# Kernel optimization log

Hardware: AMD Instinct MI355X
Metric: run time of the kernel (lower is better)

Reference implementation:

```python
import jax, jax.numpy as jnp
import numpy as np

B, S, F = 4, 2048, 64
HID, D, H = 256, 128, 8
DK = D // H


def _mlp_params(key, fan_in, hid, out):
    k1, k2, k3, k4 = jax.random.split(key, 4)
    s1 = 1.0 / np.sqrt(fan_in)
    s2 = 1.0 / np.sqrt(hid)
    return (
        jax.random.uniform(k1, (fan_in, hid), jnp.float32, -s1, s1),
        jax.random.uniform(k2, (hid,), jnp.float32, -s1, s1),
        jax.random.uniform(k3, (hid, out), jnp.float32, -s2, s2),
        jax.random.uniform(k4, (out,), jnp.float32, -s2, s2),
    )


def setup_inputs() -> dict:
    key = jax.random.key(0)
    kx, kq, kk, kv = jax.random.split(key, 4)
    qW1, qb1, qW2, qb2 = _mlp_params(kq, F, HID, D)
    kW1, kb1, kW2, kb2 = _mlp_params(kk, F, HID, D)
    vW1, vb1, vW2, vb2 = _mlp_params(kv, F, HID, D)
    return {
        "x": jax.random.normal(kx, (B, S, F), jnp.float32),
        "qW1": qW1, "qb1": qb1, "qW2": qW2, "qb2": qb2,
        "kW1": kW1, "kb1": kb1, "kW2": kW2, "kb2": kb2,
        "vW1": vW1, "vb1": vb1, "vW2": vW2, "vb2": vb2,
    }


def _mlp(x, W1, b1, W2, b2):
    h = jax.nn.elu(x @ W1 + b1)
    return h @ W2 + b2


def reference(x, qW1, qb1, qW2, qb2, kW1, kb1, kW2, kb2, vW1, vb1, vW2, vb2):
    b = x.shape[0]
    q = _mlp(x, qW1, qb1, qW2, qb2).reshape(b, -1, H, DK)  # [B,S,H,dk]
    k = _mlp(x, kW1, kb1, kW2, kb2).reshape(b, -1, H, DK)
    v = _mlp(x, vW1, vb1, vW2, vb2).reshape(b, -1, H, DK)
    scores = jnp.einsum("bqhd,bkhd->bhqk", q, k) / np.sqrt(DK).astype(np.float32)
    attn = jax.nn.softmax(scores, axis=-1)
    out = jnp.einsum("bhqk,bkhd->bqhd", attn, v).reshape(b, -1, D)  # [B,S,D]
    return jnp.max(out, axis=1)  # [B,D]
```

## Files before the change

kernel.cpp:

```cpp
#include <hip/hip_runtime.h>
#include <hip/hip_bf16.h>
#include <math.h>
#include <string.h>

#define BB 4
#define SS 2048
#define FF 64
#define HID 256
#define DD 128
#define HH 8
#define DK 16
#define NROWS (BB*SS)
#define MROWS 32
#define QPB 64
#define NQB (SS/QPB)
#define KSPLIT 4
#define KRANGE (SS/KSPLIT)
#define XSTR 72
#define HSTR 264
#define VROWS 17

#define QSCALE 0.3606737602222409f

typedef __attribute__((ext_vector_type(8))) short short8;
typedef __attribute__((ext_vector_type(16))) float float16v;

static __device__ __forceinline__ unsigned pk_bf16(float a, float b) {
    __hip_bfloat16 ha = __float2bfloat16(a), hb = __float2bfloat16(b);
    unsigned short lo, hi;
    memcpy(&lo, &ha, 2); memcpy(&hi, &hb, 2);
    return ((unsigned)hi << 16) | (unsigned)lo;
}
static __device__ __forceinline__ unsigned trunc_pk(float a, float b) {
    return __builtin_amdgcn_perm(__float_as_uint(b), __float_as_uint(a), 0x07060302u);
}

__global__ __launch_bounds__(256) void convert_kernel(
    const float* __restrict__ qW1, const float* __restrict__ kW1, const float* __restrict__ vW1,
    const float* __restrict__ qW2, const float* __restrict__ kW2, const float* __restrict__ vW2,
    __hip_bfloat16* __restrict__ W1T, __hip_bfloat16* __restrict__ W2T)
{
    const int m = blockIdx.x;
    const int quarter = blockIdx.y;
    const int t = threadIdx.x;
    if (m < 3) {
        const float* src = (m == 0) ? qW1 : (m == 1) ? kW1 : vW1;
        __hip_bfloat16* dst = W1T + (size_t)m * (FF * HID);
        const int c = t;
        for (int k0 = quarter * 16; k0 < quarter * 16 + 16; k0 += 8) {
            float v[8];
            #pragma unroll
            for (int j = 0; j < 8; ++j) v[j] = src[(size_t)(k0 + j) * HID + c];
            uint4 u = make_uint4(pk_bf16(v[0], v[1]), pk_bf16(v[2], v[3]),
                                 pk_bf16(v[4], v[5]), pk_bf16(v[6], v[7]));
            *(uint4*)&dst[(size_t)c * FF + k0] = u;
        }
    } else {
        const float* src = (m == 3) ? qW2 : (m == 4) ? kW2 : vW2;
        __hip_bfloat16* dst = W2T + (size_t)(m - 3) * (HID * DD);
        const int c = t & 127;
        const int half = t >> 7;
        const int kb = quarter * 64 + half * 32;
        for (int k0 = kb; k0 < kb + 32; k0 += 8) {
            float v[8];
            #pragma unroll
            for (int j = 0; j < 8; ++j) v[j] = src[(size_t)(k0 + j) * DD + c];
            uint4 u = make_uint4(pk_bf16(v[0], v[1]), pk_bf16(v[2], v[3]),
                                 pk_bf16(v[4], v[5]), pk_bf16(v[6], v[7]));
            *(uint4*)&dst[(size_t)c * HID + k0] = u;
        }
    }
}

__global__ __launch_bounds__(256, 3) void mlp_kernel(
    const float* __restrict__ x,
    const float* __restrict__ qb1, const float* __restrict__ kb1, const float* __restrict__ vb1,
    const float* __restrict__ qb2, const float* __restrict__ kb2, const float* __restrict__ vb2,
    const __hip_bfloat16* __restrict__ W1T, const __hip_bfloat16* __restrict__ W2T,
    __hip_bfloat16* __restrict__ Qb, __hip_bfloat16* __restrict__ Kb,
    __hip_bfloat16* __restrict__ Vt)
{
    const int blk   = blockIdx.x;
    const int which = blockIdx.y;
    const int t     = threadIdx.x;
    const int w     = t >> 6;
    const int lane  = t & 63;
    const int n     = lane & 31;
    const int hg    = lane >> 5;
    const int row0  = blk * MROWS;
    const int b     = row0 >> 11;
    const int s0    = row0 & (SS - 1);

    const float* b1 = (which == 0) ? qb1 : (which == 1) ? kb1 : vb1;
    const float* b2 = (which == 0) ? qb2 : (which == 1) ? kb2 : vb2;
    const __hip_bfloat16* W1m = W1T + (size_t)which * (FF * HID);
    const __hip_bfloat16* W2m = W2T + (size_t)which * (HID * DD);

    __shared__ __hip_bfloat16 smem[MROWS * HSTR];

    {
        const int r  = t >> 3;
        const int k0 = (t & 7) * 8;
        const float* xp = x + (size_t)(row0 + r) * FF + k0;
        float4 a0 = *(const float4*)xp;
        float4 a1 = *(const float4*)(xp + 4);
        uint4 u = make_uint4(pk_bf16(a0.x, a0.y), pk_bf16(a0.z, a0.w),
                             pk_bf16(a1.x, a1.y), pk_bf16(a1.z, a1.w));
        *(uint4*)&smem[r * XSTR + k0] = u;
    }
    __syncthreads();

    short8 afr[4];
    #pragma unroll
    for (int s = 0; s < 4; ++s)
        afr[s] = *(const short8*)&smem[n * XSTR + 16 * s + 8 * hg];

    const int c0a = w * 64, c0b = w * 64 + 32;
    float16v acc0, acc1;
    {
        const float bia = b1[c0a + n], bib = b1[c0b + n];
        #pragma unroll
        for (int i = 0; i < 16; ++i) { acc0[i] = bia; acc1[i] = bib; }
    }
    #pragma unroll
    for (int s = 0; s < 4; ++s) {
        const short8 bf0 = *(const short8*)&W1m[(size_t)(c0a + n) * FF + 16 * s + 8 * hg];
        const short8 bf1 = *(const short8*)&W1m[(size_t)(c0b + n) * FF + 16 * s + 8 * hg];
        acc0 = __builtin_amdgcn_mfma_f32_32x32x16_bf16(afr[s], bf0, acc0, 0, 0, 0);
        acc1 = __builtin_amdgcn_mfma_f32_32x32x16_bf16(afr[s], bf1, acc1, 0, 0, 0);
    }
    #pragma unroll
    for (int i = 0; i < 16; ++i) {
        const float v0 = acc0[i], v1 = acc1[i];
        acc0[i] = (v0 > 0.f) ? v0 : expm1f(v0);
        acc1[i] = (v1 > 0.f) ? v1 : expm1f(v1);
    }
    __syncthreads();

    #pragma unroll
    for (int r = 0; r < 16; ++r) {
        const int q = (r & 3) + 8 * (r >> 2) + 4 * hg;
        smem[q * HSTR + c0a + n] = __float2bfloat16(acc0[r]);
        smem[q * HSTR + c0b + n] = __float2bfloat16(acc1[r]);
    }
    __syncthreads();

    const int c2 = w * 32;
    float16v acc;
    {
        const float bi = b2[c2 + n];
        #pragma unroll
        for (int i = 0; i < 16; ++i) acc[i] = bi;
    }
    #pragma unroll 4
    for (int s = 0; s < 16; ++s) {
        const short8 af = *(const short8*)&smem[n * HSTR + 16 * s + 8 * hg];
        const short8 bf = *(const short8*)&W2m[(size_t)(c2 + n) * HID + 16 * s + 8 * hg];
        acc = __builtin_amdgcn_mfma_f32_32x32x16_bf16(af, bf, acc, 0, 0, 0);
    }

    const int col = c2 + n;
    const int hh  = col >> 4;
    const int dk0 = col & 15;
    const int bh  = b * HH + hh;
    if (which < 2) {
        const float sc = (which == 0) ? QSCALE : 1.0f;
        __hip_bfloat16* dst = (which == 0) ? Qb : Kb;
        #pragma unroll
        for (int r = 0; r < 16; ++r) {
            const int q = (r & 3) + 8 * (r >> 2) + 4 * hg;
            dst[((size_t)bh * SS + s0 + q) * DK + dk0] = __float2bfloat16(acc[r] * sc);
        }
    } else {
        __hip_bfloat16* vrow = Vt + ((size_t)bh * VROWS + dk0) * SS;
        #pragma unroll
        for (int r2 = 0; r2 < 4; ++r2) {
            const int s = s0 + 8 * r2 + 4 * hg;
            uint2 u = make_uint2(pk_bf16(acc[4 * r2 + 0], acc[4 * r2 + 1]),
                                 pk_bf16(acc[4 * r2 + 2], acc[4 * r2 + 3]));
            *(uint2*)&vrow[s] = u;
        }
        const int hh2 = t >> 5, sl = t & 31;
        Vt[((size_t)(b * HH + hh2) * VROWS + 16) * SS + s0 + sl] = __float2bfloat16(1.0f);
    }
}

__global__ __launch_bounds__(512, 8) void attn_kernel(
    const __hip_bfloat16* __restrict__ Qb,
    const __hip_bfloat16* __restrict__ Kb,
    const __hip_bfloat16* __restrict__ Vt,
    float* __restrict__ partial)
{
    const int qblk = blockIdx.x;
    const int h    = blockIdx.y;
    const int b    = blockIdx.z;
    const int bh   = b * HH + h;
    const int t    = threadIdx.x;
    const int w    = t >> 6;
    const int lane = t & 63;
    const int qt   = w >> 2;
    const int sp   = w & 3;
    const int n    = lane & 31;
    const int hg   = lane >> 5;

    __shared__ float sO[8][32][DK];
    __shared__ float sL[8][32];
    __shared__ float sV[QPB][DK];
    __shared__ float sM2[8][DK];

    const size_t bh_s = (size_t)bh * SS;
    const int q0 = qblk * QPB + qt * 32;

    const short8 qf = *(const short8*)(Qb + (bh_s + q0 + n) * DK + hg * 8);

    const __hip_bfloat16* kptr = Kb + (bh_s + sp * KRANGE) * DK + hg * 8;
    const int vd = (n < 16) ? n : 16;
    const __hip_bfloat16* vptr = Vt + ((size_t)bh * VROWS + vd) * SS + sp * KRANGE + hg * 8;

    float16v acc;
    #pragma unroll
    for (int i = 0; i < 16; ++i) acc[i] = 0.f;

    for (int kb = 0; kb < KRANGE; kb += 32) {
        const short8 kf  = *(const short8*)(kptr + (size_t)(kb + n) * DK);
        const short8 vf0 = *(const short8*)(vptr + kb);
        const short8 vf1 = *(const short8*)(vptr + kb + 16);

        float16v z;
        #pragma unroll
        for (int i = 0; i < 16; ++i) z[i] = 0.f;
        const float16v st = __builtin_amdgcn_mfma_f32_32x32x16_bf16(kf, qf, z, 0, 0, 0);

        unsigned P[8];
        #pragma unroll
        for (int j = 0; j < 8; ++j)
            P[j] = trunc_pk(exp2f(st[2 * j]), exp2f(st[2 * j + 1]));

        const int e0 = __shfl_xor((int)P[0], 32, 64);
        const int e1 = __shfl_xor((int)P[1], 32, 64);
        const int e2 = __shfl_xor((int)P[2], 32, 64);
        const int e3 = __shfl_xor((int)P[3], 32, 64);
        const int e4 = __shfl_xor((int)P[4], 32, 64);
        const int e5 = __shfl_xor((int)P[5], 32, 64);
        const int e6 = __shfl_xor((int)P[6], 32, 64);
        const int e7 = __shfl_xor((int)P[7], 32, 64);

        union { int i4[4]; short8 s8; } A1, A2;
        const bool hiHalf = (hg != 0);
        A1.i4[0] = hiHalf ? e2 : (int)P[0];
        A1.i4[1] = hiHalf ? e3 : (int)P[1];
        A1.i4[2] = hiHalf ? (int)P[2] : e0;
        A1.i4[3] = hiHalf ? (int)P[3] : e1;
        A2.i4[0] = hiHalf ? e6 : (int)P[4];
        A2.i4[1] = hiHalf ? e7 : (int)P[5];
        A2.i4[2] = hiHalf ? (int)P[6] : e4;
        A2.i4[3] = hiHalf ? (int)P[7] : e5;

        acc = __builtin_amdgcn_mfma_f32_32x32x16_bf16(A1.s8, vf0, acc, 0, 0, 0);
        acc = __builtin_amdgcn_mfma_f32_32x32x16_bf16(A2.s8, vf1, acc, 0, 0, 0);
    }

    if (n < 16) {
        #pragma unroll
        for (int r = 0; r < 16; ++r) {
            const int q = (r & 3) + 8 * (r >> 2) + 4 * hg;
            sO[w][q][n] = acc[r];
        }
    } else if (n == 16) {
        #pragma unroll
        for (int r = 0; r < 16; ++r) {
            const int q = (r & 3) + 8 * (r >> 2) + 4 * hg;
            sL[w][q] = acc[r];
        }
    }
    __syncthreads();

    for (int it = t; it < QPB * DK; it += 512) {
        const int qt2 = it >> 9;
        const int q   = (it >> 4) & 31;
        const int d   = it & 15;
        const int w0  = qt2 * 4;
        const float Ov = sO[w0][q][d] + sO[w0+1][q][d] + sO[w0+2][q][d] + sO[w0+3][q][d];
        const float Lv = sL[w0][q] + sL[w0+1][q] + sL[w0+2][q] + sL[w0+3][q];
        sV[qt2 * 32 + q][d] = Ov / Lv;
    }
    __syncthreads();

    if (t < 128) {
        const int d = t & 15, g = t >> 4;
        float mx = sV[g * 8][d];
        #pragma unroll
        for (int i = 1; i < 8; ++i) mx = fmaxf(mx, sV[g * 8 + i][d]);
        sM2[g][d] = mx;
    }
    __syncthreads();

    if (t < DK) {
        float mx = sM2[0][t];
        #pragma unroll
        for (int g = 1; g < 8; ++g) mx = fmaxf(mx, sM2[g][t]);
        partial[((size_t)bh * NQB + qblk) * DK + t] = mx;
    }
}

__global__ void reduce_kernel(const float* __restrict__ partial,
                              float* __restrict__ out)
{
    const int g   = blockIdx.x * 256 + threadIdx.x;
    const int b   = g >> 7;
    const int col = g & 127;
    const int h   = col >> 4;
    const int d   = col & 15;
    float m = -1e30f;
    #pragma unroll
    for (int c = 0; c < NQB; ++c)
        m = fmaxf(m, partial[((size_t)(b * HH + h) * NQB + c) * DK + d]);
    out[g] = m;
}

extern "C" void kernel_launch(void* const* d_in, const int* in_sizes, int n_in,
                              void* d_out, int out_size, void* d_ws, size_t ws_size,
                              hipStream_t stream)
{
    const float* x   = (const float*)d_in[0];
    const float* qW1 = (const float*)d_in[1];
    const float* qb1 = (const float*)d_in[2];
    const float* qW2 = (const float*)d_in[3];
    const float* qb2 = (const float*)d_in[4];
    const float* kW1 = (const float*)d_in[5];
    const float* kb1 = (const float*)d_in[6];
    const float* kW2 = (const float*)d_in[7];
    const float* kb2 = (const float*)d_in[8];
    const float* vW1 = (const float*)d_in[9];
    const float* vb1 = (const float*)d_in[10];
    const float* vW2 = (const float*)d_in[11];
    const float* vb2 = (const float*)d_in[12];

    char* ws = (char*)d_ws;
    __hip_bfloat16* Qb  = (__hip_bfloat16*)(ws);
    __hip_bfloat16* Kb  = (__hip_bfloat16*)(ws + (size_t)2 * 1024 * 1024);
    __hip_bfloat16* Vt  = (__hip_bfloat16*)(ws + (size_t)4 * 1024 * 1024);
    __hip_bfloat16* W1T = (__hip_bfloat16*)(ws + (size_t)6400 * 1024);
    __hip_bfloat16* W2T = (__hip_bfloat16*)(ws + (size_t)6528 * 1024);
    float* partial      = (float*)(ws + (size_t)6784 * 1024);

    convert_kernel<<<dim3(6, 4), 256, 0, stream>>>(qW1, kW1, vW1, qW2, kW2, vW2, W1T, W2T);

    mlp_kernel<<<dim3(NROWS / MROWS, 3), 256, 0, stream>>>(
        x, qb1, kb1, vb1, qb2, kb2, vb2, W1T, W2T, Qb, Kb, Vt);

    attn_kernel<<<dim3(NQB, HH, BB), 512, 0, stream>>>(Qb, Kb, Vt, partial);

    reduce_kernel<<<2, 256, 0, stream>>>(partial, (float*)d_out);
}
```

Before: 130.0 us.

## Transpose MFMA operand roles to remove cross-lane shuffles in attention

In the attention kernel, the PV matmul now consumes the exp'd score fragment directly in its MFMA output layout. It permutes the K dimension by loading V with strided 4-element loads instead of doing eight cross-half shuffles and selects per iteration. The MLP kernel swaps A/B operands so outputs are row-major per lane, which enables packed bf16 stores and vectorized bias loads. It also uses __expf for ELU and drops the occupancy hint. This trades the shuffle and select work for narrower V loads and slightly lower ELU precision.

After: 136.5 us. 5.0% more time.

```diff
diff --git a/kernel.cpp b/kernel.cpp
--- a/kernel.cpp
+++ b/kernel.cpp
@@ -72,7 +72,7 @@
     }
 }
 
-__global__ __launch_bounds__(256, 3) void mlp_kernel(
+__global__ __launch_bounds__(256) void mlp_kernel(
     const float* __restrict__ x,
     const float* __restrict__ qb1, const float* __restrict__ kb1, const float* __restrict__ vb1,
     const float* __restrict__ qb2, const float* __restrict__ kb2, const float* __restrict__ vb2,
@@ -110,75 +110,78 @@
     }
     __syncthreads();
 
-    short8 afr[4];
-    #pragma unroll
-    for (int s = 0; s < 4; ++s)
-        afr[s] = *(const short8*)&smem[n * XSTR + 16 * s + 8 * hg];
-
     const int c0a = w * 64, c0b = w * 64 + 32;
     float16v acc0, acc1;
     {
-        const float bia = b1[c0a + n], bib = b1[c0b + n];
-        #pragma unroll
-        for (int i = 0; i < 16; ++i) { acc0[i] = bia; acc1[i] = bib; }
+        #pragma unroll
+        for (int g = 0; g < 4; ++g) {
+            const float4 ba = *(const float4*)&b1[c0a + 8 * g + 4 * hg];
+            const float4 bb = *(const float4*)&b1[c0b + 8 * g + 4 * hg];
+            acc0[4*g+0] = ba.x; acc0[4*g+1] = ba.y; acc0[4*g+2] = ba.z; acc0[4*g+3] = ba.w;
+            acc1[4*g+0] = bb.x; acc1[4*g+1] = bb.y; acc1[4*g+2] = bb.z; acc1[4*g+3] = bb.w;
+        }
     }
     #pragma unroll
     for (int s = 0; s < 4; ++s) {
-        const short8 bf0 = *(const short8*)&W1m[(size_t)(c0a + n) * FF + 16 * s + 8 * hg];
-        const short8 bf1 = *(const short8*)&W1m[(size_t)(c0b + n) * FF + 16 * s + 8 * hg];
-        acc0 = __builtin_amdgcn_mfma_f32_32x32x16_bf16(afr[s], bf0, acc0, 0, 0, 0);
-        acc1 = __builtin_amdgcn_mfma_f32_32x32x16_bf16(afr[s], bf1, acc1, 0, 0, 0);
+        const short8 xf = *(const short8*)&smem[n * XSTR + 16 * s + 8 * hg];
+        const short8 a0 = *(const short8*)&W1m[(size_t)(c0a + n) * FF + 16 * s + 8 * hg];
+        const short8 a1 = *(const short8*)&W1m[(size_t)(c0b + n) * FF + 16 * s + 8 * hg];
+        acc0 = __builtin_amdgcn_mfma_f32_32x32x16_bf16(a0, xf, acc0, 0, 0, 0);
+        acc1 = __builtin_amdgcn_mfma_f32_32x32x16_bf16(a1, xf, acc1, 0, 0, 0);
     }
     #pragma unroll
     for (int i = 0; i < 16; ++i) {
         const float v0 = acc0[i], v1 = acc1[i];
-        acc0[i] = (v0 > 0.f) ? v0 : expm1f(v0);
-        acc1[i] = (v1 > 0.f) ? v1 : expm1f(v1);
-    }
-    __syncthreads();
-
-    #pragma unroll
-    for (int r = 0; r < 16; ++r) {
-        const int q = (r & 3) + 8 * (r >> 2) + 4 * hg;
-        smem[q * HSTR + c0a + n] = __float2bfloat16(acc0[r]);
-        smem[q * HSTR + c0b + n] = __float2bfloat16(acc1[r]);
-    }
-    __syncthreads();
-
-    const int c2 = w * 32;
+        acc0[i] = (v0 > 0.f) ? v0 : (__expf(v0) - 1.f);
+        acc1[i] = (v1 > 0.f) ? v1 : (__expf(v1) - 1.f);
+    }
+    __syncthreads();
+
+    #pragma unroll
+    for (int g = 0; g < 4; ++g) {
+        const int ca = c0a + 8 * g + 4 * hg;
+        const int cb = c0b + 8 * g + 4 * hg;
+        *(unsigned*)&smem[n * HSTR + ca]     = pk_bf16(acc0[4*g+0], acc0[4*g+1]);
+        *(unsigned*)&smem[n * HSTR + ca + 2] = pk_bf16(acc0[4*g+2], acc0[4*g+3]);
+        *(unsigned*)&smem[n * HSTR + cb]     = pk_bf16(acc1[4*g+0], acc1[4*g+1]);
+        *(unsigned*)&smem[n * HSTR + cb + 2] = pk_bf16(acc1[4*g+2], acc1[4*g+3]);
+    }
+    __syncthreads();
+
+    const int d0 = w * 32;
     float16v acc;
-    {
-        const float bi = b2[c2 + n];
-        #pragma unroll
-        for (int i = 0; i < 16; ++i) acc[i] = bi;
+    #pragma unroll
+    for (int g = 0; g < 4; ++g) {
+        const float4 bv = *(const float4*)&b2[d0 + 8 * g + 4 * hg];
+        acc[4*g+0] = bv.x; acc[4*g+1] = bv.y; acc[4*g+2] = bv.z; acc[4*g+3] = bv.w;
     }
     #pragma unroll 4
     for (int s = 0; s < 16; ++s) {
-        const short8 af = *(const short8*)&smem[n * HSTR + 16 * s + 8 * hg];
-        const short8 bf = *(const short8*)&W2m[(size_t)(c2 + n) * HID + 16 * s + 8 * hg];
-        acc = __builtin_amdgcn_mfma_f32_32x32x16_bf16(af, bf, acc, 0, 0, 0);
-    }
-
-    const int col = c2 + n;
-    const int hh  = col >> 4;
-    const int dk0 = col & 15;
-    const int bh  = b * HH + hh;
+        const short8 hf = *(const short8*)&smem[n * HSTR + 16 * s + 8 * hg];
+        const short8 af = *(const short8*)&W2m[(size_t)(d0 + n) * HID + 16 * s + 8 * hg];
+        acc = __builtin_amdgcn_mfma_f32_32x32x16_bf16(af, hf, acc, 0, 0, 0);
+    }
+
     if (which < 2) {
         const float sc = (which == 0) ? QSCALE : 1.0f;
         __hip_bfloat16* dst = (which == 0) ? Qb : Kb;
         #pragma unroll
+        for (int g = 0; g < 4; ++g) {
+            const int d  = d0 + 8 * g + 4 * hg;
+            const int hh = d >> 4;
+            const int dk = d & 15;
+            const size_t base = ((size_t)(b * HH + hh) * SS + s0 + n) * DK + dk;
+            uint2 u = make_uint2(pk_bf16(acc[4*g+0] * sc, acc[4*g+1] * sc),
+                                 pk_bf16(acc[4*g+2] * sc, acc[4*g+3] * sc));
+            *(uint2*)&dst[base] = u;
+        }
+    } else {
+        #pragma unroll
         for (int r = 0; r < 16; ++r) {
-            const int q = (r & 3) + 8 * (r >> 2) + 4 * hg;
-            dst[((size_t)bh * SS + s0 + q) * DK + dk0] = __float2bfloat16(acc[r] * sc);
-        }
-    } else {
-        __hip_bfloat16* vrow = Vt + ((size_t)bh * VROWS + dk0) * SS;
-        #pragma unroll
-        for (int r2 = 0; r2 < 4; ++r2) {
-            const int s = s0 + 8 * r2 + 4 * hg;
-            uint2 u = make_uint2(pk_bf16(acc[4 * r2 + 0], acc[4 * r2 + 1]),
-                                 pk_bf16(acc[4 * r2 + 2], acc[4 * r2 + 3]));
-            *(uint2*)&vrow[s] = u;
+            const int d  = d0 + 8 * (r >> 2) + 4 * hg + (r & 3);
+            const int hh = d >> 4;
+            const int dv = d & 15;
+            Vt[((size_t)(b * HH + hh) * VROWS + dv) * SS + s0 + n] = __float2bfloat16(acc[r]);
         }
         const int hh2 = t >> 5, sl = t & 31;
         Vt[((size_t)(b * HH + hh2) * VROWS + 16) * SS + s0 + sl] = __float2bfloat16(1.0f);
@@ -215,49 +218,36 @@
 
     const __hip_bfloat16* kptr = Kb + (bh_s + sp * KRANGE) * DK + hg * 8;
     const int vd = (n < 16) ? n : 16;
-    const __hip_bfloat16* vptr = Vt + ((size_t)bh * VROWS + vd) * SS + sp * KRANGE + hg * 8;
+    const __hip_bfloat16* vptr = Vt + ((size_t)bh * VROWS + vd) * SS + sp * KRANGE + 4 * hg;
 
     float16v acc;
     #pragma unroll
     for (int i = 0; i < 16; ++i) acc[i] = 0.f;
+    float16v z;
+    #pragma unroll
+    for (int i = 0; i < 16; ++i) z[i] = 0.f;
 
     for (int kb = 0; kb < KRANGE; kb += 32) {
-        const short8 kf  = *(const short8*)(kptr + (size_t)(kb + n) * DK);
-        const short8 vf0 = *(const short8*)(vptr + kb);
-        const short8 vf1 = *(const short8*)(vptr + kb + 16);
-
-        float16v z;
-        #pragma unroll
-        for (int i = 0; i < 16; ++i) z[i] = 0.f;
+        const short8 kf = *(const short8*)(kptr + (size_t)(kb + n) * DK);
+
+        union { uint2 u2[2]; short8 s8; } B1, B2;
+        B1.u2[0] = *(const uint2*)(vptr + kb);
+        B1.u2[1] = *(const uint2*)(vptr + kb + 8);
+        B2.u2[0] = *(const uint2*)(vptr + kb + 16);
+        B2.u2[1] = *(const uint2*)(vptr + kb + 24);
+
         const float16v st = __builtin_amdgcn_mfma_f32_32x32x16_bf16(kf, qf, z, 0, 0, 0);
 
-        unsigned P[8];
-        #pragma unroll
-        for (int j = 0; j < 8; ++j)
-            P[j] = trunc_pk(exp2f(st[2 * j]), exp2f(st[2 * j + 1]));
-
-        const int e0 = __shfl_xor((int)P[0], 32, 64);
-        const int e1 = __shfl_xor((int)P[1], 32, 64);
-        const int e2 = __shfl_xor((int)P[2], 32, 64);
-        const int e3 = __shfl_xor((int)P[3], 32, 64);
-        const int e4 = __shfl_xor((int)P[4], 32, 64);
-        const int e5 = __shfl_xor((int)P[5], 32, 64);
-        const int e6 = __shfl_xor((int)P[6], 32, 64);
-        const int e7 = __shfl_xor((int)P[7], 32, 64);
-
-        union { int i4[4]; short8 s8; } A1, A2;
-        const bool hiHalf = (hg != 0);
-        A1.i4[0] = hiHalf ? e2 : (int)P[0];
-        A1.i4[1] = hiHalf ? e3 : (int)P[1];
-        A1.i4[2] = hiHalf ? (int)P[2] : e0;
-        A1.i4[3] = hiHalf ? (int)P[3] : e1;
-        A2.i4[0] = hiHalf ? e6 : (int)P[4];
-        A2.i4[1] = hiHalf ? e7 : (int)P[5];
-        A2.i4[2] = hiHalf ? (int)P[6] : e4;
-        A2.i4[3] = hiHalf ? (int)P[7] : e5;
-
-        acc = __builtin_amdgcn_mfma_f32_32x32x16_bf16(A1.s8, vf0, acc, 0, 0, 0);
-        acc = __builtin_amdgcn_mfma_f32_32x32x16_bf16(A2.s8, vf1, acc, 0, 0, 0);
+        union { unsigned u[4]; short8 s8; } A1, A2;
+        #pragma unroll
+        for (int j = 0; j < 4; ++j)
+            A1.u[j] = trunc_pk(exp2f(st[2 * j]),     exp2f(st[2 * j + 1]));
+        #pragma unroll
+        for (int j = 0; j < 4; ++j)
+            A2.u[j] = trunc_pk(exp2f(st[2 * j + 8]), exp2f(st[2 * j + 9]));
+
+        acc = __builtin_amdgcn_mfma_f32_32x32x16_bf16(A1.s8, B1.s8, acc, 0, 0, 0);
+        acc = __builtin_amdgcn_mfma_f32_32x32x16_bf16(A2.s8, B2.s8, acc, 0, 0, 0);
     }
 
     if (n < 16) {
```
